# Kernel tuning notes

Measured on AMD Instinct MI355X. Metric: run time of the kernel, lower is better.

The kernel has to match this reference:

```python
import jax, jax.numpy as jnp
import numpy as np

B, S, D = 2, 2048, 1024
H, HD = 16, 64          # num_heads, head_dim
K = 32                  # JL n_components


def setup_inputs() -> dict:
    key = jax.random.key(0)
    k1, k2, k3, k4 = jax.random.split(key, 4)
    return {
        "hidden_states": jax.random.normal(k1, (B, S, D), dtype=jnp.float32),
        "W_attn": jax.random.normal(k2, (D, 3 * D), dtype=jnp.float32) * 0.02,
        "b_attn": jnp.zeros((3 * D,), dtype=jnp.float32),
        "S_proj": jax.random.normal(k3, (K, HD), dtype=jnp.float32) / np.sqrt(K),
        "W_proj": jax.random.normal(k4, (D, D), dtype=jnp.float32) * 0.02,
        "b_proj": jnp.zeros((D,), dtype=jnp.float32),
    }


def reference(hidden_states, W_attn, b_attn, S_proj, W_proj, b_proj):
    b, s, d = hidden_states.shape
    # GPT2 Conv1D: x @ W + b, then split into q,k,v
    qkv = hidden_states @ W_attn + b_attn            # [B,S,3D]
    q, k, v = jnp.split(qkv, 3, axis=-1)
    # split heads -> [B,H,S,HD]
    def split_heads(x):
        return x.reshape(b, s, H, HD).transpose(0, 2, 1, 3)
    q = split_heads(q) @ S_proj.T                    # [B,H,S,K] JL-reduced
    k = split_heads(k) @ S_proj.T                    # [B,H,S,K]
    v = split_heads(v)                               # [B,H,S,HD]
    # naive attention: scale by sqrt(value head_dim) per GPT2 _attn
    scores = jnp.einsum("bhqk,bhsk->bhqs", q, k) / jnp.sqrt(
        jnp.asarray(HD, dtype=v.dtype))              # [B,H,S,S]
    causal = jnp.tril(jnp.ones((s, s), dtype=bool))
    mask_value = jnp.finfo(scores.dtype).min
    scores = jnp.where(causal, scores, mask_value)
    attn = jax.nn.softmax(scores, axis=-1)
    out = jnp.einsum("bhqs,bhsd->bhqd", attn, v)     # [B,H,S,HD]
    out = out.transpose(0, 2, 1, 3).reshape(b, s, d)  # merge heads
    return out @ W_proj + b_proj
```

## Files before the change

kernel.cpp:

```cpp
#include <hip/hip_runtime.h>
#include <hip/hip_bf16.h>
#include <stdint.h>

#define B_ 2
#define S_ 2048
#define D_ 1024
#define H_ 16
#define HD_ 64
#define KJL 32
#define N3 3072
#define N2 2048

typedef __attribute__((ext_vector_type(8))) __bf16 bf16x8;
typedef __attribute__((ext_vector_type(4))) float floatx4;
typedef __attribute__((ext_vector_type(4))) short short4v;
typedef __attribute__((ext_vector_type(2))) unsigned int uint2v;

__device__ __forceinline__ unsigned short f2b(float x) {
  union { float f; unsigned u; } v; v.f = x;
  unsigned r = v.u + 0x7fffu + ((v.u >> 16) & 1u);
  return (unsigned short)(r >> 16);
}

__device__ __forceinline__ unsigned int pkbf(float lo, float hi) {
  union { float f; unsigned u; } a, b;
  a.f = lo; b.f = hi;
  return __builtin_amdgcn_perm(b.u + 0x8000u, a.u + 0x8000u, 0x07060302u);
}

__device__ __forceinline__ void async16(const void* g, void* l) {
  __builtin_amdgcn_global_load_lds((__attribute__((address_space(1))) void*)(g),
                                   (__attribute__((address_space(3))) void*)(l),
                                   16, 0, 0);
}

__global__ __launch_bounds__(256)
void prep_kernel(const float* __restrict__ hidden, unsigned short* __restrict__ hB,
                 const float* __restrict__ W_attn, const float* __restrict__ b_attn,
                 const float* __restrict__ Sp, const float* __restrict__ W_proj,
                 unsigned short* __restrict__ Bt2, unsigned short* __restrict__ WpT,
                 float* __restrict__ bias2) {
  __shared__ float shmem[2048];
  const int bid = blockIdx.x;
  const int tid = threadIdx.x;

  if (bid < 512) {
    const int n4 = (B_ * S_ * D_) / 4;
    int i = bid * 256 + tid;
    for (; i < n4; i += 512 * 256) {
      float4 v = *(const float4*)(hidden + 4 * (size_t)i);
      short4v o = {(short)f2b(v.x), (short)f2b(v.y), (short)f2b(v.z), (short)f2b(v.w)};
      *(short4v*)(hB + 4 * (size_t)i) = o;
    }
  } else if (bid < 2560) {
    const float* in;
    unsigned short* out;
    int Cs, local;
    if (bid < 1536) { local = bid - 512;  in = W_attn + 2048; out = Bt2 + 1024 * 1024; Cs = N3; }
    else            { local = bid - 1536; in = W_proj;        out = WpT;               Cs = D_; }
    float (*t)[33] = (float(*)[33])shmem;
    int c0 = (local & 31) * 32, r0 = (local >> 5) * 32;
    int tx = tid & 31, ty = tid >> 5;
    for (int j = 0; j < 32; j += 8)
      t[ty + j][tx] = in[(size_t)(r0 + ty + j) * Cs + c0 + tx];
    __syncthreads();
    for (int j = 0; j < 32; j += 8)
      out[(size_t)(c0 + ty + j) * D_ + r0 + tx] = f2b(t[tx][ty + j]);
  } else {
    const int lb = bid - 2560;
    const int part = lb >> 6;
    const int h = (lb >> 2) & 15;
    const int dc = lb & 3;
    for (int i = tid; i < 32 * 64; i += 256) shmem[i] = Sp[i];
    __syncthreads();
    const float scale = part ? 1.0f : 0.125f * 1.44269504f;
    const int d = dc * 256 + tid;
    float w[64];
    const float* src = W_attn + (size_t)d * N3 + part * D_ + h * 64;
    for (int j = 0; j < 16; ++j) {
      float4 v = *(const float4*)&src[j * 4];
      w[j * 4 + 0] = v.x; w[j * 4 + 1] = v.y; w[j * 4 + 2] = v.z; w[j * 4 + 3] = v.w;
    }
    const int nbase = part * 512 + h * 32;
    for (int kjl = 0; kjl < 32; ++kjl) {
      float acc = 0.f;
      for (int hd = 0; hd < 64; ++hd) acc += w[hd] * shmem[kjl * 64 + hd];
      Bt2[(size_t)(nbase + kjl) * D_ + d] = f2b(acc * scale);
    }
    if (dc == 0 && tid < 32) {
      float acc = 0.f;
      for (int hd = 0; hd < 64; ++hd) acc += b_attn[part * D_ + h * 64 + hd] * shmem[tid * 64 + hd];
      bias2[nbase + tid] = acc * scale;
    }
  }
}

__global__ __launch_bounds__(256, 2)
void qkv2_gemm_kernel(const unsigned short* __restrict__ A,
                      const unsigned short* __restrict__ Bt,
                      const float* __restrict__ b_attn,
                      const float* __restrict__ bias2,
                      unsigned short* __restrict__ Qjl,
                      unsigned short* __restrict__ Kjl,
                      unsigned short* __restrict__ Vc) {
  __shared__ __align__(16) unsigned short As[128 * 32];
  __shared__ __align__(16) unsigned short Bs[128 * 32];
  const int tid = threadIdx.x;
  const int lane = tid & 63, wv = tid >> 6;
  const int quad = lane >> 4, col = lane & 15;
  const int wm = wv >> 1, wn = wv & 1;
  const int m0 = blockIdx.y * 128, n0 = blockIdx.x * 128;

  floatx4 acc[4][4] = {};

  for (int kk = 0; kk < D_; kk += 32) {
    for (int it = 0; it < 2; ++it) {
      int c = it * 256 + tid;
      int row = c >> 2, k8 = (c & 3) << 3;
      async16(A + (size_t)(m0 + row) * D_ + kk + k8, &As[c * 8]);
      async16(Bt + (size_t)(n0 + row) * D_ + kk + k8, &Bs[c * 8]);
    }
    asm volatile("s_waitcnt vmcnt(0)" ::: "memory");
    __syncthreads();
    bf16x8 af[4], bfr[4];
    for (int mt = 0; mt < 4; ++mt)
      af[mt] = *(const bf16x8*)&As[(wm * 64 + mt * 16 + col) * 32 + quad * 8];
    for (int nt = 0; nt < 4; ++nt)
      bfr[nt] = *(const bf16x8*)&Bs[(wn * 64 + nt * 16 + col) * 32 + quad * 8];
    for (int mt = 0; mt < 4; ++mt)
      for (int nt = 0; nt < 4; ++nt)
        acc[mt][nt] = __builtin_amdgcn_mfma_f32_16x16x32_bf16(
            af[mt], bfr[nt], acc[mt][nt], 0, 0, 0);
    __syncthreads();
  }

  const int pq = n0 >> 9;
  for (int mt = 0; mt < 4; ++mt) {
    int gm0 = m0 + wm * 64 + mt * 16 + quad * 4;
    int b = gm0 >> 11, s = gm0 & (S_ - 1);
    for (int nt = 0; nt < 4; ++nt) {
      int gn = n0 + wn * 64 + nt * 16 + col;
      if (pq >= 2) {
        int vcol = gn - 1024;
        float bs = b_attn[2048 + vcol];
        int h = vcol >> 6, hd = vcol & 63;
        short4v vv;
        for (int i = 0; i < 4; ++i)
          vv[i] = (short)f2b(acc[mt][nt][i] + bs);
        size_t idx = ((((size_t)(b * H_ + h) * 64 + (s >> 5)) * 64 + hd) * 32 + (s & 31));
        *(short4v*)&Vc[idx] = vv;
      } else {
        float bs = bias2[gn];
        int gl = gn & 511;
        int h = gl >> 5, kjl = gl & 31;
        unsigned short* dst = pq ? Kjl : Qjl;
        size_t base = ((size_t)(b * H_ + h) * S_ + s) * KJL + kjl;
        for (int i = 0; i < 4; ++i)
          dst[base + (size_t)i * KJL] = f2b(acc[mt][nt][i] + bs);
      }
    }
  }
}

__global__ __launch_bounds__(256, 2)
void attn_kernel(const unsigned short* __restrict__ Qjl,
                 const unsigned short* __restrict__ Kjl,
                 const unsigned short* __restrict__ Vc,
                 unsigned short* __restrict__ AO) {
  __shared__ __align__(16) unsigned short Ps[4][32 * 136];
  const int tid = threadIdx.x;
  const int lane = tid & 63, wv = tid >> 6;
  const int quad = lane >> 4, l15 = lane & 15;

  const int blk = blockIdx.x;
  const int xcd = blk & 7;
  const int u = blk >> 3;
  const int bhl = (u >> 4) & 3;
  const int g0 = u & 15;
  const int g = (u & 32) ? (15 - g0) : g0;
  const int bh = xcd * 4 + bhl;
  const int t = 63 - (g * 4 + wv);
  const int b = bh >> 4, h = bh & 15;

  unsigned short* Pw = &Ps[wv][0];
  const int laneK = l15 * KJL + quad * 8;
  const int laneV = l15 * 32 + quad * 8;
  const unsigned short* Kp = Kjl + (size_t)bh * S_ * KJL + laneK;
  const unsigned short* Vp = Vc + (size_t)bh * (64 * 64 * 32) + laneV;

  bf16x8 aq[2];
  for (int qn = 0; qn < 2; ++qn)
    aq[qn] = *(const bf16x8*)&Qjl[(size_t)(bh * S_ + t * 32 + qn * 16 + l15) * KJL + quad * 8];

  floatx4 o[4][2] = {};
  floatx4 psum[2] = {};
  const floatx4 zz = {0.f, 0.f, 0.f, 0.f};

  const int lastc = t >> 2;
  const int r = t & 3;

  for (int kt = 0; kt <= lastc; ++kt) {
    bf16x8 ak[8];
    for (int sm = 0; sm < 8; ++sm)
      ak[sm] = *(const bf16x8*)&Kp[sm * (16 * KJL)];
    bf16x8 bv[4][4];
    for (int ks = 0; ks < 4; ++ks)
      for (int md = 0; md < 4; ++md)
        bv[ks][md] = *(const bf16x8*)&Vp[ks * 2048 + md * 512];
    Kp += 128 * KJL;
    Vp += 8192;

    floatx4 sc[8][2];
    for (int sm = 0; sm < 8; ++sm)
      for (int qn = 0; qn < 2; ++qn)
        sc[sm][qn] = __builtin_amdgcn_mfma_f32_16x16x32_bf16(ak[sm], aq[qn], zz, 0, 0, 0);

    if (kt == lastc) {
      for (int qn = 0; qn < 2; ++qn) {
        int qloc = r * 32 + qn * 16 + l15;
        for (int sm = 0; sm < 8; ++sm)
          for (int i = 0; i < 4; ++i)
            if (sm * 16 + quad * 4 + i > qloc) sc[sm][qn][i] = -1e30f;
      }
    }

    for (int qn = 0; qn < 2; ++qn) {
      for (int sm = 0; sm < 8; ++sm) {
        float p0 = __builtin_amdgcn_exp2f(sc[sm][qn][0]);
        float p1 = __builtin_amdgcn_exp2f(sc[sm][qn][1]);
        float p2 = __builtin_amdgcn_exp2f(sc[sm][qn][2]);
        float p3 = __builtin_amdgcn_exp2f(sc[sm][qn][3]);
        psum[qn][0] += p0; psum[qn][1] += p1;
        psum[qn][2] += p2; psum[qn][3] += p3;
        uint2v pk2 = {pkbf(p0, p1), pkbf(p2, p3)};
        *(uint2v*)&Pw[(qn * 16 + l15) * 136 + sm * 16 + quad * 4] = pk2;
      }
    }

    for (int ks = 0; ks < 4; ++ks) {
      bf16x8 bp[2];
      for (int qn = 0; qn < 2; ++qn)
        bp[qn] = *(const bf16x8*)&Pw[(qn * 16 + l15) * 136 + ks * 32 + quad * 8];
      for (int qn = 0; qn < 2; ++qn)
        for (int md = 0; md < 4; ++md)
          o[md][qn] = __builtin_amdgcn_mfma_f32_16x16x32_bf16(bv[ks][md], bp[qn], o[md][qn], 0, 0, 0);
    }
  }

  for (int qn = 0; qn < 2; ++qn) {
    float l = psum[qn][0] + psum[qn][1] + psum[qn][2] + psum[qn][3];
    l += __shfl_xor(l, 16, 64);
    l += __shfl_xor(l, 32, 64);
    float inv = 1.f / l;
    for (int md = 0; md < 4; ++md) {
      uint2v t4 = {pkbf(o[md][qn][0] * inv, o[md][qn][1] * inv),
                   pkbf(o[md][qn][2] * inv, o[md][qn][3] * inv)};
      *(uint2v*)&Pw[(qn * 16 + l15) * 72 + md * 16 + quad * 4] = t4;
    }
  }
  {
    int q = lane >> 1, half = lane & 1;
    size_t gbase = ((size_t)(b * S_ + t * 32 + q)) * D_ + h * HD_ + half * 32;
    for (int jj = 0; jj < 4; ++jj) {
      bf16x8 v = *(const bf16x8*)&Pw[q * 72 + half * 32 + jj * 8];
      *(bf16x8*)&AO[gbase + jj * 8] = v;
    }
  }
}

__global__ __launch_bounds__(256, 2)
void proj_gemm_kernel(const unsigned short* __restrict__ A,
                      const unsigned short* __restrict__ Bt,
                      const float* __restrict__ bias,
                      float* __restrict__ out) {
  __shared__ __align__(16) unsigned short As[64 * 32];
  __shared__ __align__(16) unsigned short Bs[128 * 32];
  const int tid = threadIdx.x;
  const int lane = tid & 63, wv = tid >> 6;
  const int quad = lane >> 4, col = lane & 15;
  const int wm = wv >> 1, wn = wv & 1;
  const int m0 = blockIdx.y * 64, n0 = blockIdx.x * 128;

  floatx4 acc[2][4] = {};

  for (int kk = 0; kk < D_; kk += 32) {
    {
      int c = tid;
      int row = c >> 2, k8 = (c & 3) << 3;
      async16(A + (size_t)(m0 + row) * D_ + kk + k8, &As[c * 8]);
    }
    for (int it = 0; it < 2; ++it) {
      int c = it * 256 + tid;
      int row = c >> 2, k8 = (c & 3) << 3;
      async16(Bt + (size_t)(n0 + row) * D_ + kk + k8, &Bs[c * 8]);
    }
    asm volatile("s_waitcnt vmcnt(0)" ::: "memory");
    __syncthreads();
    bf16x8 af[2], bfr[4];
    for (int mt = 0; mt < 2; ++mt)
      af[mt] = *(const bf16x8*)&As[(wm * 32 + mt * 16 + col) * 32 + quad * 8];
    for (int nt = 0; nt < 4; ++nt)
      bfr[nt] = *(const bf16x8*)&Bs[(wn * 64 + nt * 16 + col) * 32 + quad * 8];
    for (int mt = 0; mt < 2; ++mt)
      for (int nt = 0; nt < 4; ++nt)
        acc[mt][nt] = __builtin_amdgcn_mfma_f32_16x16x32_bf16(
            af[mt], bfr[nt], acc[mt][nt], 0, 0, 0);
    __syncthreads();
  }

  for (int mt = 0; mt < 2; ++mt) {
    int gm0 = m0 + wm * 32 + mt * 16 + quad * 4;
    for (int nt = 0; nt < 4; ++nt) {
      int gn = n0 + wn * 64 + nt * 16 + col;
      float bs = bias[gn];
      for (int i = 0; i < 4; ++i)
        out[(size_t)(gm0 + i) * D_ + gn] = acc[mt][nt][i] + bs;
    }
  }
}

extern "C" void kernel_launch(void* const* d_in, const int* in_sizes, int n_in,
                              void* d_out, int out_size, void* d_ws, size_t ws_size,
                              hipStream_t stream) {
  (void)in_sizes; (void)n_in; (void)out_size; (void)ws_size;
  const float* hidden = (const float*)d_in[0];
  const float* W_attn = (const float*)d_in[1];
  const float* b_attn = (const float*)d_in[2];
  const float* S_proj = (const float*)d_in[3];
  const float* W_proj = (const float*)d_in[4];
  const float* b_proj = (const float*)d_in[5];
  float* out = (float*)d_out;

  char* ws = (char*)d_ws;
  unsigned short* hB    = (unsigned short*)(ws);
  unsigned short* Bt2   = (unsigned short*)(ws + (8u << 20));
  unsigned short* WpT   = (unsigned short*)(ws + (12u << 20));
  float*          bias2 = (float*)         (ws + (14u << 20));
  unsigned short* Qjl   = (unsigned short*)(ws + (15u << 20));
  unsigned short* Kjl   = (unsigned short*)(ws + (19u << 20));
  unsigned short* Vc    = (unsigned short*)(ws + (23u << 20));
  unsigned short* AO    = (unsigned short*)(ws + (31u << 20));

  prep_kernel<<<2688, 256, 0, stream>>>(hidden, hB, W_attn, b_attn, S_proj,
                                        W_proj, Bt2, WpT, bias2);
  qkv2_gemm_kernel<<<dim3(N2 / 128, (B_ * S_) / 128), 256, 0, stream>>>(
      hB, Bt2, b_attn, bias2, Qjl, Kjl, Vc);
  attn_kernel<<<512, 256, 0, stream>>>(Qjl, Kjl, Vc, AO);
  proj_gemm_kernel<<<dim3(D_ / 128, (B_ * S_) / 64), 256, 0, stream>>>(
      AO, WpT, b_proj, out);
}
```

Before: 187.6 us.

## Split attention KV range across two blocks with merge kernel; widen GEMM K-step

The attention kernel now splits each query tile's causal key range into two halves handled by separate blocks. Each half writes unnormalized fp32 partial outputs and row sums to a workspace, and a new merge kernel adds them, normalizes, and writes the bf16 head output. This is meant to double parallelism and balance the causal workload, at the cost of an extra launch and fp32 partial traffic. Separately, both GEMMs now load 64-wide K chunks per barrier pair to halve synchronization count, using twice the LDS.

After: 298.3 us. 59.0% more time.

```diff
diff --git a/kernel.cpp b/kernel.cpp
--- a/kernel.cpp
+++ b/kernel.cpp
@@ -103,8 +103,8 @@
                       unsigned short* __restrict__ Qjl,
                       unsigned short* __restrict__ Kjl,
                       unsigned short* __restrict__ Vc) {
-  __shared__ __align__(16) unsigned short As[128 * 32];
-  __shared__ __align__(16) unsigned short Bs[128 * 32];
+  __shared__ __align__(16) unsigned short As[2][128 * 32];
+  __shared__ __align__(16) unsigned short Bs[2][128 * 32];
   const int tid = threadIdx.x;
   const int lane = tid & 63, wv = tid >> 6;
   const int quad = lane >> 4, col = lane & 15;
@@ -113,24 +113,32 @@
 
   floatx4 acc[4][4] = {};
 
-  for (int kk = 0; kk < D_; kk += 32) {
-    for (int it = 0; it < 2; ++it) {
+  for (int kk = 0; kk < D_; kk += 64) {
+    for (int it = 0; it < 4; ++it) {
       int c = it * 256 + tid;
-      int row = c >> 2, k8 = (c & 3) << 3;
-      async16(A + (size_t)(m0 + row) * D_ + kk + k8, &As[c * 8]);
-      async16(Bt + (size_t)(n0 + row) * D_ + kk + k8, &Bs[c * 8]);
+      int ks = c >> 9, row = (c >> 2) & 127, kc = c & 3;
+      async16(A + (size_t)(m0 + row) * D_ + kk + ks * 32 + kc * 8,
+              (unsigned short*)As + c * 8);
+    }
+    for (int it = 0; it < 4; ++it) {
+      int c = it * 256 + tid;
+      int ks = c >> 9, row = (c >> 2) & 127, kc = c & 3;
+      async16(Bt + (size_t)(n0 + row) * D_ + kk + ks * 32 + kc * 8,
+              (unsigned short*)Bs + c * 8);
     }
     asm volatile("s_waitcnt vmcnt(0)" ::: "memory");
     __syncthreads();
-    bf16x8 af[4], bfr[4];
-    for (int mt = 0; mt < 4; ++mt)
-      af[mt] = *(const bf16x8*)&As[(wm * 64 + mt * 16 + col) * 32 + quad * 8];
-    for (int nt = 0; nt < 4; ++nt)
-      bfr[nt] = *(const bf16x8*)&Bs[(wn * 64 + nt * 16 + col) * 32 + quad * 8];
-    for (int mt = 0; mt < 4; ++mt)
+    for (int ks = 0; ks < 2; ++ks) {
+      bf16x8 af[4], bfr[4];
+      for (int mt = 0; mt < 4; ++mt)
+        af[mt] = *(const bf16x8*)&As[ks][(wm * 64 + mt * 16 + col) * 32 + quad * 8];
       for (int nt = 0; nt < 4; ++nt)
-        acc[mt][nt] = __builtin_amdgcn_mfma_f32_16x16x32_bf16(
-            af[mt], bfr[nt], acc[mt][nt], 0, 0, 0);
+        bfr[nt] = *(const bf16x8*)&Bs[ks][(wn * 64 + nt * 16 + col) * 32 + quad * 8];
+      for (int mt = 0; mt < 4; ++mt)
+        for (int nt = 0; nt < 4; ++nt)
+          acc[mt][nt] = __builtin_amdgcn_mfma_f32_16x16x32_bf16(
+              af[mt], bfr[nt], acc[mt][nt], 0, 0, 0);
+    }
     __syncthreads();
   }
 
@@ -162,31 +170,34 @@
   }
 }
 
-__global__ __launch_bounds__(256, 2)
+__global__ __launch_bounds__(256, 4)
 void attn_kernel(const unsigned short* __restrict__ Qjl,
                  const unsigned short* __restrict__ Kjl,
                  const unsigned short* __restrict__ Vc,
-                 unsigned short* __restrict__ AO) {
+                 float* __restrict__ Part) {
   __shared__ __align__(16) unsigned short Ps[4][32 * 136];
   const int tid = threadIdx.x;
   const int lane = tid & 63, wv = tid >> 6;
   const int quad = lane >> 4, l15 = lane & 15;
 
   const int blk = blockIdx.x;
-  const int xcd = blk & 7;
-  const int u = blk >> 3;
-  const int bhl = (u >> 4) & 3;
-  const int g0 = u & 15;
-  const int g = (u & 32) ? (15 - g0) : g0;
-  const int bh = xcd * 4 + bhl;
+  const int bh = blk & 31;
+  const int g0 = (blk >> 5) & 7;
+  const int half = (blk >> 8) & 1;
+  const int g = (blk & 512) ? (15 - g0) : g0;
   const int t = 63 - (g * 4 + wv);
-  const int b = bh >> 4, h = bh & 15;
 
   unsigned short* Pw = &Ps[wv][0];
+  const int lastc = t >> 2;
+  const int nch = lastc + 1;
+  const int kb = half ? ((nch + 1) >> 1) : 0;
+  const int ke = half ? nch : ((nch + 1) >> 1);
+  const int r = t & 3;
+
   const int laneK = l15 * KJL + quad * 8;
   const int laneV = l15 * 32 + quad * 8;
-  const unsigned short* Kp = Kjl + (size_t)bh * S_ * KJL + laneK;
-  const unsigned short* Vp = Vc + (size_t)bh * (64 * 64 * 32) + laneV;
+  const unsigned short* Kp = Kjl + (size_t)bh * S_ * KJL + laneK + (size_t)kb * 128 * KJL;
+  const unsigned short* Vp = Vc + (size_t)bh * (64 * 64 * 32) + laneV + (size_t)kb * 8192;
 
   bf16x8 aq[2];
   for (int qn = 0; qn < 2; ++qn)
@@ -196,10 +207,7 @@
   floatx4 psum[2] = {};
   const floatx4 zz = {0.f, 0.f, 0.f, 0.f};
 
-  const int lastc = t >> 2;
-  const int r = t & 3;
-
-  for (int kt = 0; kt <= lastc; ++kt) {
+  for (int kt = kb; kt < ke; ++kt) {
     bf16x8 ak[8];
     for (int sm = 0; sm < 8; ++sm)
       ak[sm] = *(const bf16x8*)&Kp[sm * (16 * KJL)];
@@ -247,22 +255,54 @@
     }
   }
 
+  float l0 = psum[0][0] + psum[0][1] + psum[0][2] + psum[0][3];
+  float l1 = psum[1][0] + psum[1][1] + psum[1][2] + psum[1][3];
+  l0 += __shfl_xor(l0, 16, 64); l0 += __shfl_xor(l0, 32, 64);
+  l1 += __shfl_xor(l1, 16, 64); l1 += __shfl_xor(l1, 32, 64);
+
+  const int tile = bh * 64 + t;
+  float* Pp = Part + ((size_t)(tile * 2 + half) * 9 * 64 + lane) * 4;
+  for (int qn = 0; qn < 2; ++qn)
+    for (int md = 0; md < 4; ++md)
+      *(floatx4*)(Pp + (size_t)(qn * 4 + md) * 256) = o[md][qn];
+  floatx4 lv = {l0, l1, 0.f, 0.f};
+  *(floatx4*)(Pp + (size_t)8 * 256) = lv;
+}
+
+__global__ __launch_bounds__(256, 4)
+void merge_kernel(const float* __restrict__ Part, unsigned short* __restrict__ AO) {
+  __shared__ __align__(16) unsigned short Os[4][32 * 72];
+  const int tid = threadIdx.x;
+  const int lane = tid & 63, wv = tid >> 6;
+  const int quad = lane >> 4, l15 = lane & 15;
+  const int tile = blockIdx.x * 4 + wv;
+  const int bh = tile >> 6, t = tile & 63;
+  const int b = bh >> 4, h = bh & 15;
+
+  const float* P0 = Part + ((size_t)(tile * 2 + 0) * 9 * 64 + lane) * 4;
+  const float* P1 = Part + ((size_t)(tile * 2 + 1) * 9 * 64 + lane) * 4;
+  floatx4 la = *(const floatx4*)(P0 + (size_t)8 * 256);
+  floatx4 lb = *(const floatx4*)(P1 + (size_t)8 * 256);
+  float inv0 = 1.f / (la[0] + lb[0]);
+  float inv1 = 1.f / (la[1] + lb[1]);
+
+  unsigned short* Pw = &Os[wv][0];
   for (int qn = 0; qn < 2; ++qn) {
-    float l = psum[qn][0] + psum[qn][1] + psum[qn][2] + psum[qn][3];
-    l += __shfl_xor(l, 16, 64);
-    l += __shfl_xor(l, 32, 64);
-    float inv = 1.f / l;
+    float inv = qn ? inv1 : inv0;
     for (int md = 0; md < 4; ++md) {
-      uint2v t4 = {pkbf(o[md][qn][0] * inv, o[md][qn][1] * inv),
-                   pkbf(o[md][qn][2] * inv, o[md][qn][3] * inv)};
+      floatx4 a = *(const floatx4*)(P0 + (size_t)(qn * 4 + md) * 256);
+      floatx4 c = *(const floatx4*)(P1 + (size_t)(qn * 4 + md) * 256);
+      uint2v t4 = {pkbf((a[0] + c[0]) * inv, (a[1] + c[1]) * inv),
+                   pkbf((a[2] + c[2]) * inv, (a[3] + c[3]) * inv)};
       *(uint2v*)&Pw[(qn * 16 + l15) * 72 + md * 16 + quad * 4] = t4;
     }
   }
+  asm volatile("s_waitcnt lgkmcnt(0)" ::: "memory");
   {
-    int q = lane >> 1, half = lane & 1;
-    size_t gbase = ((size_t)(b * S_ + t * 32 + q)) * D_ + h * HD_ + half * 32;
+    int q = lane >> 1, hf = lane & 1;
+    size_t gbase = ((size_t)(b * S_ + t * 32 + q)) * D_ + h * HD_ + hf * 32;
     for (int jj = 0; jj < 4; ++jj) {
-      bf16x8 v = *(const bf16x8*)&Pw[q * 72 + half * 32 + jj * 8];
+      bf16x8 v = *(const bf16x8*)&Pw[q * 72 + hf * 32 + jj * 8];
       *(bf16x8*)&AO[gbase + jj * 8] = v;
     }
   }
@@ -273,8 +313,8 @@
                       const unsigned short* __restrict__ Bt,
                       const float* __restrict__ bias,
                       float* __restrict__ out) {
-  __shared__ __align__(16) unsigned short As[64 * 32];
-  __shared__ __align__(16) unsigned short Bs[128 * 32];
+  __shared__ __align__(16) unsigned short As[2][64 * 32];
+  __shared__ __align__(16) unsigned short Bs[2][128 * 32];
   const int tid = threadIdx.x;
   const int lane = tid & 63, wv = tid >> 6;
   const int quad = lane >> 4, col = lane & 15;
@@ -283,28 +323,32 @@
 
   floatx4 acc[2][4] = {};
 
-  for (int kk = 0; kk < D_; kk += 32) {
-    {
-      int c = tid;
-      int row = c >> 2, k8 = (c & 3) << 3;
-      async16(A + (size_t)(m0 + row) * D_ + kk + k8, &As[c * 8]);
-    }
+  for (int kk = 0; kk < D_; kk += 64) {
     for (int it = 0; it < 2; ++it) {
       int c = it * 256 + tid;
-      int row = c >> 2, k8 = (c & 3) << 3;
-      async16(Bt + (size_t)(n0 + row) * D_ + kk + k8, &Bs[c * 8]);
+      int ks = c >> 8, row = (c >> 2) & 63, kc = c & 3;
+      async16(A + (size_t)(m0 + row) * D_ + kk + ks * 32 + kc * 8,
+              (unsigned short*)As + c * 8);
+    }
+    for (int it = 0; it < 4; ++it) {
+      int c = it * 256 + tid;
+      int ks = c >> 9, row = (c >> 2) & 127, kc = c & 3;
+      async16(Bt + (size_t)(n0 + row) * D_ + kk + ks * 32 + kc * 8,
+              (unsigned short*)Bs + c * 8);
     }
     asm volatile("s_waitcnt vmcnt(0)" ::: "memory");
     __syncthreads();
-    bf16x8 af[2], bfr[4];
-    for (int mt = 0; mt < 2; ++mt)
-      af[mt] = *(const bf16x8*)&As[(wm * 32 + mt * 16 + col) * 32 + quad * 8];
-    for (int nt = 0; nt < 4; ++nt)
-      bfr[nt] = *(const bf16x8*)&Bs[(wn * 64 + nt * 16 + col) * 32 + quad * 8];
-    for (int mt = 0; mt < 2; ++mt)
+    for (int ks = 0; ks < 2; ++ks) {
+      bf16x8 af[2], bfr[4];
+      for (int mt = 0; mt < 2; ++mt)
+        af[mt] = *(const bf16x8*)&As[ks][(wm * 32 + mt * 16 + col) * 32 + quad * 8];
       for (int nt = 0; nt < 4; ++nt)
-        acc[mt][nt] = __builtin_amdgcn_mfma_f32_16x16x32_bf16(
-            af[mt], bfr[nt], acc[mt][nt], 0, 0, 0);
+        bfr[nt] = *(const bf16x8*)&Bs[ks][(wn * 64 + nt * 16 + col) * 32 + quad * 8];
+      for (int mt = 0; mt < 2; ++mt)
+        for (int nt = 0; nt < 4; ++nt)
+          acc[mt][nt] = __builtin_amdgcn_mfma_f32_16x16x32_bf16(
+              af[mt], bfr[nt], acc[mt][nt], 0, 0, 0);
+    }
     __syncthreads();
   }
 
@@ -340,12 +384,14 @@
   unsigned short* Kjl   = (unsigned short*)(ws + (19u << 20));
   unsigned short* Vc    = (unsigned short*)(ws + (23u << 20));
   unsigned short* AO    = (unsigned short*)(ws + (31u << 20));
+  float*          Part  = (float*)         (ws + (40u << 20));
 
   prep_kernel<<<2688, 256, 0, stream>>>(hidden, hB, W_attn, b_attn, S_proj,
                                         W_proj, Bt2, WpT, bias2);
   qkv2_gemm_kernel<<<dim3(N2 / 128, (B_ * S_) / 128), 256, 0, stream>>>(
       hB, Bt2, b_attn, bias2, Qjl, Kjl, Vc);
-  attn_kernel<<<512, 256, 0, stream>>>(Qjl, Kjl, Vc, AO);
+  attn_kernel<<<1024, 256, 0, stream>>>(Qjl, Kjl, Vc, Part);
+  merge_kernel<<<512, 256, 0, stream>>>(Part, AO);
   proj_gemm_kernel<<<dim3(D_ / 128, (B_ * S_) / 64), 256, 0, stream>>>(
       AO, WpT, b_proj, out);
 }
```
